# Performance work log

Hardware: AMD Instinct MI355X
Metric: run time of the kernel (lower is better)

## Reference

```python
import jax, jax.numpy as jnp
import numpy as np

B = 16384
IN_DIM = 1280
BELLY = 1024   # int(scale_dim * belly_expand)
SCALE = 512
NBINS = 100
NPAT = 10
TAU = 0.25
BASE = 3.0
LEVELS = 12


def setup_inputs() -> dict:
    key = jax.random.key(0)
    ks = jax.random.split(key, 10)
    def w(i, shape, fan_in):
        return jax.random.normal(ks[i], shape, jnp.float32) * (0.5 / np.sqrt(fan_in))
    return {
        "features": jax.random.normal(ks[0], (B, IN_DIM), jnp.float32),
        "timesteps": jax.random.randint(ks[1], (B,), 0, 1000, jnp.int32),
        "W1": w(2, (IN_DIM, BELLY), IN_DIM),
        "b1": jnp.zeros((BELLY,), jnp.float32),
        "W2": w(3, (BELLY, SCALE), BELLY),            # no bias (bias=False)
        "Wt": w(4, (SCALE, NBINS), SCALE),
        "bt": jnp.zeros((NBINS,), jnp.float32),
        "Wp": w(5, (SCALE, NBINS * NPAT), SCALE),
        "bp": jnp.zeros((NBINS * NPAT,), jnp.float32),
        "w_pos": w(6, (SCALE, 1), SCALE),             # cantor feature_to_position
        "b_pos": jnp.zeros((1,), jnp.float32),
        "alpha": jnp.float32(0.5),
    }


def cantor_staircase(z, positions, w_pos, b_pos, alpha):
    # z: [B, SCALE] normalized features; positions: [B] int timestep bins
    centers = jnp.array([0.5, 1.5, 2.5], jnp.float32)
    max_pos = positions.max() + 1
    denom = jnp.maximum(max_pos - 1, 1).astype(jnp.float32)
    pos_f = positions.astype(jnp.float32)
    x_base = jnp.where(max_pos > 1, pos_f / denom, pos_f)
    x_base = jnp.clip(x_base, 1e-6, 1.0 - 1e-6)
    shift = jnp.tanh((z @ w_pos)[:, 0] + b_pos[0]) * 0.3
    x0 = jnp.clip(x_base + shift, 1e-6, 1.0 - 1e-6)

    def step(carry, _):
        x, Cx, w = carry
        y = x * BASE                                   # [B]
        logits = -((y[:, None] - centers) ** 2) / (TAU + 1e-8)  # [B,3]
        p = jax.nn.softmax(logits, axis=-1)
        bit = p[:, 1] * alpha + p[:, 2]
        Cx = Cx + bit * w
        x = y - jnp.floor(y)
        return (x, Cx, w * 0.5), None

    (x, Cx, w), _ = jax.lax.scan(step, (x0, jnp.zeros_like(x0), jnp.float32(0.5)), None, length=LEVELS)
    return jnp.clip(Cx, 0.0, 1.0)


def reference(features, timesteps, W1, b1, W2, Wt, bt, Wp, bp, w_pos, b_pos, alpha):
    # projection: Linear -> ReLU -> (dropout=identity at eval) -> Linear(no bias)
    h = jax.nn.relu(features @ W1 + b1)                # [B, BELLY]
    z = h @ W2                                         # [B, SCALE]
    z = z / jnp.maximum(jnp.linalg.norm(z, axis=-1, keepdims=True), 1e-12)
    timestep_logits = z @ Wt + bt                      # [B, NBINS]
    timestep_class = jnp.clip(
        (timesteps.astype(jnp.float32) / 1000.0 * NBINS).astype(jnp.int32), 0, NBINS - 1)
    cantor_values = cantor_staircase(z, timestep_class, w_pos, b_pos, alpha)
    pattern_logits = z @ Wp + bp                       # [B, NBINS*NPAT]
    return (z, timestep_logits, pattern_logits, timestep_class, cantor_values)
```

## Files before the change

### kernel.cpp

```cpp
#include <hip/hip_runtime.h>

#define B_ROWS 16384
#define IN_DIM 1280
#define BELLY  1024
#define SCALE  512
#define NBINS  100
#define NPTOT  1000

typedef __attribute__((ext_vector_type(8))) short short8_t;
typedef __attribute__((ext_vector_type(4))) float f32x4;

__device__ __forceinline__ unsigned short f2bf(float f) {
  union { float f; unsigned int u; } v; v.f = f;
  unsigned int r = v.u + 0x7FFFu + ((v.u >> 16) & 1u);
  return (unsigned short)(r >> 16);
}

__device__ __forceinline__ void gload16(const void* g, void* l) {
  __builtin_amdgcn_global_load_lds(
      (const __attribute__((address_space(1))) unsigned int*)g,
      (__attribute__((address_space(3))) unsigned int*)l, 16, 0, 0);
}

__global__ void cvt_f32_bf16(const float* __restrict__ in,
                             unsigned short* __restrict__ out, int n4) {
  int i = blockIdx.x * blockDim.x + threadIdx.x;
  int stride = gridDim.x * blockDim.x;
  for (; i < n4; i += stride) {
    float4 v = ((const float4*)in)[i];
    ushort4 o;
    o.x = f2bf(v.x); o.y = f2bf(v.y); o.z = f2bf(v.z); o.w = f2bf(v.w);
    ((ushort4*)out)[i] = o;
  }
}

__global__ void transpose_cvt(const float* __restrict__ in,
                              unsigned short* __restrict__ out,
                              int K, int N, int Npad) {
  __shared__ float tile[32][33];
  int k0 = blockIdx.x * 32;
  int n0 = blockIdx.y * 32;
  int tx = threadIdx.x, ty = threadIdx.y;
  #pragma unroll
  for (int r = 0; r < 32; r += 8) {
    int k = k0 + ty + r, n = n0 + tx;
    tile[ty + r][tx] = (k < K && n < N) ? in[(size_t)k * N + n] : 0.0f;
  }
  __syncthreads();
  #pragma unroll
  for (int r = 0; r < 32; r += 8) {
    int n = n0 + ty + r, k = k0 + tx;
    if (n < Npad && k < K) out[(size_t)n * K + k] = f2bf(tile[tx][ty + r]);
  }
}

__global__ void tclass_kernel(const int* __restrict__ ts, float* __restrict__ outc,
                              int* __restrict__ gmax, int n) {
  __shared__ int smax;
  if (threadIdx.x == 0) smax = 0;
  __syncthreads();
  int local = 0;
  for (int i = blockIdx.x * blockDim.x + threadIdx.x; i < n;
       i += gridDim.x * blockDim.x) {
    float v = (float)ts[i] / 1000.0f * 100.0f;
    int c = (int)v;
    c = min(max(c, 0), NBINS - 1);
    outc[i] = (float)c;
    local = max(local, c);
  }
  atomicMax(&smax, local);
  __syncthreads();
  if (threadIdx.x == 0) atomicMax(gmax, smax);
}

template<int K, int EPI>
__global__ __launch_bounds__(512, 1)
void gemm256(const unsigned short* __restrict__ A,
             const unsigned short* __restrict__ Bt,
             float* __restrict__ outF, unsigned short* __restrict__ outH,
             const float* __restrict__ bias, int Nvalid, int ldOut) {
  __shared__ __align__(16) unsigned short lds[65536];
  constexpr int NT = K / 64;
  static_assert(NT % 2 == 0, "NT must be even");
  const int tid  = threadIdx.x;
  const int wid  = tid >> 6;
  const int lane = tid & 63;
  const int r0 = blockIdx.x * 256;
  const int c0 = blockIdx.y * 256;

  const int srow = wid * 16 + (lane >> 3);
  const int scol = (((lane & 7) ^ (lane >> 3)) << 3);
  const unsigned short* gA = A  + (size_t)(r0 + srow) * K + scol;
  const unsigned short* gB = Bt + (size_t)(c0 + srow) * K + scol;
  const int sdst = wid * 1024;

  const int fr = lane & 15;
  const int Ah = wid >> 2;
  const int wc = (wid & 3) * 64;
  const int ca0 = ((((lane >> 4) << 4) +  0) ^ ((lane & 7) << 4)) >> 1;
  const int ca1 = ((((lane >> 4) << 4) + 64) ^ ((lane & 7) << 4)) >> 1;

  f32x4 acc[8][4] = {};
  short8_t af[4][2];
  short8_t bfr[2][2][2];

#define STAGE_(buf, mat, half, kt) do {                                        \
    const unsigned short* g_ = ((mat) == 0 ? gA : gB)                          \
        + (size_t)(half) * 128 * K + (size_t)(kt) * 64;                        \
    unsigned short* l_ = &lds[(buf) * 32768 + (mat) * 16384 + (half) * 8192 + sdst]; \
    gload16(g_, l_);                                                           \
    gload16(g_ + 8 * K, l_ + 512);                                             \
  } while (0)

#define LDA_(buf, mh) do {                                                     \
    const unsigned short* ab_ = &lds[(buf) * 32768 + Ah * 8192];               \
    _Pragma("unroll")                                                          \
    for (int mm = 0; mm < 4; ++mm) {                                           \
      int rwh_ = (mh) * 64 + mm * 16 + fr;                                     \
      af[mm][0] = *(const short8_t*)&ab_[rwh_ * 64 + ca0];                     \
      af[mm][1] = *(const short8_t*)&ab_[rwh_ * 64 + ca1];                     \
    } } while (0)

#define LDB_(buf, nh) do {                                                     \
    _Pragma("unroll")                                                          \
    for (int nn = 0; nn < 2; ++nn) {                                           \
      int brow_ = wc + ((nh) * 2 + nn) * 16;                                   \
      const unsigned short* bb_ = &lds[(buf) * 32768 + 16384 + (brow_ >> 7) * 8192]; \
      int rwh_ = (brow_ & 127) + fr;                                           \
      bfr[nh][nn][0] = *(const short8_t*)&bb_[rwh_ * 64 + ca0];                \
      bfr[nh][nn][1] = *(const short8_t*)&bb_[rwh_ * 64 + ca1];                \
    } } while (0)

#define MM_(mh, nh) do {                                                       \
    _Pragma("unroll")                                                          \
    for (int mm = 0; mm < 4; ++mm)                                             \
      _Pragma("unroll")                                                        \
      for (int nn = 0; nn < 2; ++nn) {                                         \
        acc[(mh)*4+mm][(nh)*2+nn] = __builtin_amdgcn_mfma_f32_16x16x32_bf16(   \
            af[mm][0], bfr[nh][nn][0], acc[(mh)*4+mm][(nh)*2+nn], 0, 0, 0);    \
        acc[(mh)*4+mm][(nh)*2+nn] = __builtin_amdgcn_mfma_f32_16x16x32_bf16(   \
            af[mm][1], bfr[nh][nn][1], acc[(mh)*4+mm][(nh)*2+nn], 0, 0, 0);    \
      } } while (0)

#define BAR_       __builtin_amdgcn_s_barrier()
#define LGKM0_     asm volatile("s_waitcnt lgkmcnt(0)")
#define VM4_       asm volatile("s_waitcnt vmcnt(4)" ::: "memory")
#define PRIO1_     __builtin_amdgcn_s_setprio(1)
#define PRIO0_     __builtin_amdgcn_s_setprio(0)

  STAGE_(0, 1, 0, 0); STAGE_(0, 1, 1, 0);
  STAGE_(0, 0, 0, 0); STAGE_(0, 0, 1, 0);
  STAGE_(1, 1, 0, 1); STAGE_(1, 1, 1, 1);
  VM4_;
  BAR_;

  for (int t = 0; t < NT; t += 2) {
    const int t2 = (t + 2) % NT;
    const int t3 = (t + 3) % NT;
    LDA_(0, 0); LDB_(0, 0); STAGE_(1, 0, 0, t + 1);
    BAR_; LGKM0_; PRIO1_; MM_(0, 0); PRIO0_; BAR_;
    LDB_(0, 1); STAGE_(1, 0, 1, t + 1);
    BAR_; LGKM0_; PRIO1_; MM_(0, 1); PRIO0_; BAR_;
    LDA_(0, 1); STAGE_(0, 1, 0, t2);
    BAR_; LGKM0_; PRIO1_; MM_(1, 0); PRIO0_; BAR_;
    STAGE_(0, 1, 1, t2); VM4_;
    BAR_; LGKM0_; PRIO1_; MM_(1, 1); PRIO0_; BAR_;
    LDA_(1, 0); LDB_(1, 0); STAGE_(0, 0, 0, t2);
    BAR_; LGKM0_; PRIO1_; MM_(0, 0); PRIO0_; BAR_;
    LDB_(1, 1); STAGE_(0, 0, 1, t2);
    BAR_; LGKM0_; PRIO1_; MM_(0, 1); PRIO0_; BAR_;
    LDA_(1, 1); STAGE_(1, 1, 0, t3);
    BAR_; LGKM0_; PRIO1_; MM_(1, 0); PRIO0_; BAR_;
    STAGE_(1, 1, 1, t3); VM4_;
    BAR_; LGKM0_; PRIO1_; MM_(1, 1); PRIO0_; BAR_;
  }

  asm volatile("s_waitcnt vmcnt(0)" ::: "memory");

  const int orow = (lane >> 4) * 4;
  const int wrr  = (wid >> 2) * 128;
  #pragma unroll
  for (int m = 0; m < 8; ++m) {
    #pragma unroll
    for (int n = 0; n < 4; ++n) {
      #pragma unroll
      for (int i = 0; i < 4; ++i) {
        int row = r0 + wrr + m * 16 + orow + i;
        int col = c0 + wc + n * 16 + fr;
        float v = acc[m][n][i];
        if (EPI == 0) {
          v += bias[col];
          v = fmaxf(v, 0.0f);
          outH[(size_t)row * ldOut + col] = f2bf(v);
        } else if (EPI == 1) {
          outF[(size_t)row * ldOut + col] = v;
        } else {
          if (col < Nvalid) outF[(size_t)row * ldOut + col] = v + bias[col];
        }
      }
    }
  }
#undef STAGE_
#undef LDA_
#undef LDB_
#undef MM_
}

template<int K, int EPI>
__global__ __launch_bounds__(256)
void gemm128(const unsigned short* __restrict__ A,
             const unsigned short* __restrict__ Bt,
             float* __restrict__ outF, unsigned short* __restrict__ outH,
             const float* __restrict__ bias, int Nvalid, int ldOut) {
  __shared__ __align__(16) unsigned short As[128 * 32];
  __shared__ __align__(16) unsigned short Bs[128 * 32];

  const int tid  = threadIdx.x;
  const int wid  = tid >> 6;
  const int lane = tid & 63;
  const int r0 = blockIdx.x * 128;
  const int c0 = blockIdx.y * 128;

  const int arow = lane >> 2;
  const int acol = (lane & 3) * 8;
  const unsigned short* gA0 = A  + (size_t)(r0 + 16 * (2 * wid + 0) + arow) * K + acol;
  const unsigned short* gA1 = A  + (size_t)(r0 + 16 * (2 * wid + 1) + arow) * K + acol;
  const unsigned short* gB0 = Bt + (size_t)(c0 + 16 * (2 * wid + 0) + arow) * K + acol;
  const unsigned short* gB1 = Bt + (size_t)(c0 + 16 * (2 * wid + 1) + arow) * K + acol;
  unsigned short* lA0 = &As[(2 * wid + 0) * 512];
  unsigned short* lA1 = &As[(2 * wid + 1) * 512];
  unsigned short* lB0 = &Bs[(2 * wid + 0) * 512];
  unsigned short* lB1 = &Bs[(2 * wid + 1) * 512];

  const int wr   = (wid >> 1) * 64;
  const int wc   = (wid & 1) * 64;
  const int fr   = lane & 15;
  const int koff = (lane >> 4) * 8;

  f32x4 acc[4][4] = {};

  for (int k0 = 0; k0 < K; k0 += 32) {
    gload16(gA0 + k0, lA0);
    gload16(gA1 + k0, lA1);
    gload16(gB0 + k0, lB0);
    gload16(gB1 + k0, lB1);
    __syncthreads();

    short8_t af[4], bfr[4];
    #pragma unroll
    for (int m = 0; m < 4; ++m)
      af[m] = *(const short8_t*)&As[(wr + m * 16 + fr) * 32 + koff];
    #pragma unroll
    for (int n = 0; n < 4; ++n)
      bfr[n] = *(const short8_t*)&Bs[(wc + n * 16 + fr) * 32 + koff];

    #pragma unroll
    for (int m = 0; m < 4; ++m)
      #pragma unroll
      for (int n = 0; n < 4; ++n)
        acc[m][n] = __builtin_amdgcn_mfma_f32_16x16x32_bf16(af[m], bfr[n], acc[m][n], 0, 0, 0);

    __syncthreads();
  }

  const int orow = (lane >> 4) * 4;
  #pragma unroll
  for (int m = 0; m < 4; ++m) {
    #pragma unroll
    for (int n = 0; n < 4; ++n) {
      #pragma unroll
      for (int i = 0; i < 4; ++i) {
        int row = r0 + wr + m * 16 + orow + i;
        int col = c0 + wc + n * 16 + fr;
        float v = acc[m][n][i];
        if (EPI == 0) {
          v += bias[col];
          v = fmaxf(v, 0.0f);
          outH[(size_t)row * ldOut + col] = f2bf(v);
        } else if (EPI == 1) {
          outF[(size_t)row * ldOut + col] = v;
        } else {
          if (col < Nvalid) outF[(size_t)row * ldOut + col] = v + bias[col];
        }
      }
    }
  }
}

__global__ void normalize_kernel(const float* __restrict__ zraw,
                                 float* __restrict__ zout,
                                 unsigned short* __restrict__ zb) {
  int wid = threadIdx.x >> 6, lane = threadIdx.x & 63;
  int row = blockIdx.x * 4 + wid;
  const float4* zr = (const float4*)(zraw + (size_t)row * SCALE);
  float4 v0 = zr[lane];
  float4 v1 = zr[lane + 64];
  float s = v0.x * v0.x + v0.y * v0.y + v0.z * v0.z + v0.w * v0.w
          + v1.x * v1.x + v1.y * v1.y + v1.z * v1.z + v1.w * v1.w;
  #pragma unroll
  for (int off = 1; off < 64; off <<= 1) s += __shfl_xor(s, off);
  float scale = 1.0f / fmaxf(sqrtf(s), 1e-12f);
  float4 o0, o1;
  o0.x = v0.x * scale; o0.y = v0.y * scale; o0.z = v0.z * scale; o0.w = v0.w * scale;
  o1.x = v1.x * scale; o1.y = v1.y * scale; o1.z = v1.z * scale; o1.w = v1.w * scale;
  ((float4*)(zout + (size_t)row * SCALE))[lane] = o0;
  ((float4*)(zout + (size_t)row * SCALE))[lane + 64] = o1;
  ushort4 b0, b1;
  b0.x = f2bf(o0.x); b0.y = f2bf(o0.y); b0.z = f2bf(o0.z); b0.w = f2bf(o0.w);
  b1.x = f2bf(o1.x); b1.y = f2bf(o1.y); b1.z = f2bf(o1.z); b1.w = f2bf(o1.w);
  ((ushort4*)(zb + (size_t)row * SCALE))[lane] = b0;
  ((ushort4*)(zb + (size_t)row * SCALE))[lane + 64] = b1;
}

__global__ void cantor_kernel(const float* __restrict__ z,
                              const float* __restrict__ w_pos,
                              const float* __restrict__ b_pos,
                              const float* __restrict__ alpha_p,
                              const float* __restrict__ tclassf,
                              const int* __restrict__ gmax,
                              float* __restrict__ out) {
  int wid = threadIdx.x >> 6, lane = threadIdx.x & 63;
  int row = blockIdx.x * 4 + wid;
  const float4* zr = (const float4*)(z + (size_t)row * SCALE);
  const float4* wp = (const float4*)w_pos;
  float4 a0 = zr[lane], a1 = zr[lane + 64];
  float4 c0 = wp[lane], c1 = wp[lane + 64];
  float s = a0.x * c0.x + a0.y * c0.y + a0.z * c0.z + a0.w * c0.w
          + a1.x * c1.x + a1.y * c1.y + a1.z * c1.z + a1.w * c1.w;
  #pragma unroll
  for (int off = 1; off < 64; off <<= 1) s += __shfl_xor(s, off);

  float shift = tanhf(s + b_pos[0]) * 0.3f;
  int max_pos = *gmax + 1;
  float denom = (float)max(max_pos - 1, 1);
  float posf = tclassf[row];
  float x = (max_pos > 1) ? (posf / denom) : posf;
  x = fminf(fmaxf(x, 1e-6f), 1.0f - 1e-6f);
  x = x + shift;
  x = fminf(fmaxf(x, 1e-6f), 1.0f - 1e-6f);

  float alpha = alpha_p[0];
  const float inv = 1.0f / (0.25f + 1e-8f);
  float Cx = 0.0f, w = 0.5f;
  #pragma unroll
  for (int l = 0; l < 12; ++l) {
    float y = x * 3.0f;
    float d0 = y - 0.5f, d1 = y - 1.5f, d2 = y - 2.5f;
    float l0 = -(d0 * d0) * inv, l1 = -(d1 * d1) * inv, l2 = -(d2 * d2) * inv;
    float mx = fmaxf(l0, fmaxf(l1, l2));
    float e0 = __expf(l0 - mx), e1 = __expf(l1 - mx), e2 = __expf(l2 - mx);
    float bit = (e1 * alpha + e2) / (e0 + e1 + e2);
    Cx += bit * w;
    x = y - floorf(y);
    w *= 0.5f;
  }
  if (lane == 0) out[row] = fminf(fmaxf(Cx, 0.0f), 1.0f);
}

extern "C" void kernel_launch(void* const* d_in, const int* in_sizes, int n_in,
                              void* d_out, int out_size, void* d_ws, size_t ws_size,
                              hipStream_t stream) {
  const float* features = (const float*)d_in[0];
  const int*   timesteps = (const int*)d_in[1];
  const float* W1 = (const float*)d_in[2];
  const float* b1 = (const float*)d_in[3];
  const float* W2 = (const float*)d_in[4];
  const float* Wt = (const float*)d_in[5];
  const float* bt = (const float*)d_in[6];
  const float* Wp = (const float*)d_in[7];
  const float* bp = (const float*)d_in[8];
  const float* w_pos = (const float*)d_in[9];
  const float* b_pos = (const float*)d_in[10];
  const float* alpha = (const float*)d_in[11];

  char* ws = (char*)d_ws;
  const size_t WS_H   = (size_t)B_ROWS * IN_DIM * 2;
  const size_t WS_ZB  = WS_H + (size_t)B_ROWS * BELLY * 2;
  const size_t WS_W1T = WS_ZB + (size_t)B_ROWS * SCALE * 2;
  const size_t WS_W2T = WS_W1T + (size_t)BELLY * IN_DIM * 2;
  const size_t WS_WPT = WS_W2T + (size_t)SCALE * BELLY * 2;
  const size_t WS_WTT = WS_WPT + (size_t)1024 * SCALE * 2;
  const size_t WS_MAX = WS_WTT + (size_t)128 * SCALE * 2;

  unsigned short* featB = (unsigned short*)(ws);
  float*          zraw  = (float*)(ws);
  unsigned short* hB    = (unsigned short*)(ws + WS_H);
  unsigned short* zB    = (unsigned short*)(ws + WS_ZB);
  unsigned short* W1T   = (unsigned short*)(ws + WS_W1T);
  unsigned short* W2T   = (unsigned short*)(ws + WS_W2T);
  unsigned short* WPT   = (unsigned short*)(ws + WS_WPT);
  unsigned short* WTT   = (unsigned short*)(ws + WS_WTT);
  int*            gmax  = (int*)(ws + WS_MAX);

  float* out  = (float*)d_out;
  float* o_z  = out;
  float* o_t  = o_z + (size_t)B_ROWS * SCALE;
  float* o_p  = o_t + (size_t)B_ROWS * NBINS;
  float* o_c  = o_p + (size_t)B_ROWS * NPTOT;
  float* o_cv = o_c + B_ROWS;

  hipMemsetAsync(gmax, 0, 4, stream);

  cvt_f32_bf16<<<2048, 256, 0, stream>>>(features, featB, B_ROWS * IN_DIM / 4);

  dim3 tb(32, 8);
  transpose_cvt<<<dim3(40, 32), tb, 0, stream>>>(W1, W1T, IN_DIM, BELLY, BELLY);
  transpose_cvt<<<dim3(32, 16), tb, 0, stream>>>(W2, W2T, BELLY, SCALE, SCALE);
  transpose_cvt<<<dim3(16, 32), tb, 0, stream>>>(Wp, WPT, SCALE, NPTOT, 1024);
  transpose_cvt<<<dim3(16, 4),  tb, 0, stream>>>(Wt, WTT, SCALE, NBINS, 128);

  tclass_kernel<<<64, 256, 0, stream>>>(timesteps, o_c, gmax, B_ROWS);

  gemm256<IN_DIM, 0><<<dim3(B_ROWS / 256, BELLY / 256), 512, 0, stream>>>(
      featB, W1T, nullptr, hB, b1, BELLY, BELLY);
  gemm256<BELLY, 1><<<dim3(B_ROWS / 256, SCALE / 256), 512, 0, stream>>>(
      hB, W2T, zraw, nullptr, nullptr, SCALE, SCALE);

  normalize_kernel<<<B_ROWS / 4, 256, 0, stream>>>(zraw, o_z, zB);

  gemm256<SCALE, 2><<<dim3(B_ROWS / 256, 4), 512, 0, stream>>>(
      zB, WPT, o_p, nullptr, bp, NPTOT, NPTOT);
  gemm128<SCALE, 2><<<dim3(B_ROWS / 128, 1), 256, 0, stream>>>(
      zB, WTT, o_t, nullptr, bt, NBINS, NBINS);

  cantor_kernel<<<B_ROWS / 4, 256, 0, stream>>>(o_z, w_pos, b_pos, alpha, o_c, gmax, o_cv);
}
```

Baseline: 348.6 us.

## Fuse fp32->bf16 conversion into GEMM1, merge head GEMMs and norm+cantor

The first GEMM now loads fp32 features straight into registers, converts them to bf16 and writes them to LDS, which drops the separate conversion kernel and its bf16 round trip through memory. The Wp and Wt heads are combined into one transposed weight buffer so a single 5-column-tile GEMM writes both outputs, and gemm128 is removed. Normalization and the cantor computation are fused into one kernel that reuses the raw z dot product with w_pos. The risk is that register staging with vmcnt(0) waits may hurt pipelining in GEMM1, and the padded head columns waste some MFMA work.

```diff
diff --git a/kernel.cpp b/kernel.cpp
--- a/kernel.cpp
+++ b/kernel.cpp
@@ -1,4 +1,5 @@
 #include <hip/hip_runtime.h>
+#include <hip/hip_bf16.h>
 
 #define B_ROWS 16384
 #define IN_DIM 1280
@@ -20,18 +21,6 @@
   __builtin_amdgcn_global_load_lds(
       (const __attribute__((address_space(1))) unsigned int*)g,
       (__attribute__((address_space(3))) unsigned int*)l, 16, 0, 0);
-}
-
-__global__ void cvt_f32_bf16(const float* __restrict__ in,
-                             unsigned short* __restrict__ out, int n4) {
-  int i = blockIdx.x * blockDim.x + threadIdx.x;
-  int stride = gridDim.x * blockDim.x;
-  for (; i < n4; i += stride) {
-    float4 v = ((const float4*)in)[i];
-    ushort4 o;
-    o.x = f2bf(v.x); o.y = f2bf(v.y); o.z = f2bf(v.z); o.w = f2bf(v.w);
-    ((ushort4*)out)[i] = o;
-  }
 }
 
 __global__ void transpose_cvt(const float* __restrict__ in,
@@ -73,12 +62,14 @@
   if (threadIdx.x == 0) atomicMax(gmax, smax);
 }
 
-template<int K, int EPI>
+template<int K, int EPI, bool AF32>
 __global__ __launch_bounds__(512, 1)
-void gemm256(const unsigned short* __restrict__ A,
+void gemm256(const void* __restrict__ Av,
              const unsigned short* __restrict__ Bt,
              float* __restrict__ outF, unsigned short* __restrict__ outH,
-             const float* __restrict__ bias, int Nvalid, int ldOut) {
+             const float* __restrict__ bias,
+             float* __restrict__ outF2, const float* __restrict__ bias2,
+             int ldOut) {
   __shared__ __align__(16) unsigned short lds[65536];
   constexpr int NT = K / 64;
   static_assert(NT % 2 == 0, "NT must be even");
@@ -90,9 +81,14 @@
 
   const int srow = wid * 16 + (lane >> 3);
   const int scol = (((lane & 7) ^ (lane >> 3)) << 3);
-  const unsigned short* gA = A  + (size_t)(r0 + srow) * K + scol;
   const unsigned short* gB = Bt + (size_t)(c0 + srow) * K + scol;
+  const unsigned short* gA16 = AF32 ? nullptr
+      : (const unsigned short*)Av + (size_t)(r0 + srow) * K + scol;
+  const float* gAf = AF32
+      ? (const float*)Av + (size_t)(r0 + wid * 16 + (lane >> 3)) * K + (lane & 7) * 8
+      : nullptr;
   const int sdst = wid * 1024;
+  const int swzslot = (lane & 7) ^ (lane >> 3);
 
   const int fr = lane & 15;
   const int Ah = wid >> 2;
@@ -103,14 +99,46 @@
   f32x4 acc[8][4] = {};
   short8_t af[4][2];
   short8_t bfr[2][2][2];
-
-#define STAGE_(buf, mat, half, kt) do {                                        \
-    const unsigned short* g_ = ((mat) == 0 ? gA : gB)                          \
+  float av[2][2][8];
+
+#define STAGEB_(buf, half, kt) do {                                            \
+    const unsigned short* g_ = gB                                              \
         + (size_t)(half) * 128 * K + (size_t)(kt) * 64;                        \
-    unsigned short* l_ = &lds[(buf) * 32768 + (mat) * 16384 + (half) * 8192 + sdst]; \
+    unsigned short* l_ = &lds[(buf) * 32768 + 16384 + (half) * 8192 + sdst];   \
     gload16(g_, l_);                                                           \
     gload16(g_ + 8 * K, l_ + 512);                                             \
   } while (0)
+
+#define STAGEA16_(buf, half, kt) do {                                          \
+    const unsigned short* g_ = gA16                                            \
+        + (size_t)(half) * 128 * K + (size_t)(kt) * 64;                        \
+    unsigned short* l_ = &lds[(buf) * 32768 + (half) * 8192 + sdst];           \
+    gload16(g_, l_);                                                           \
+    gload16(g_ + 8 * K, l_ + 512);                                             \
+  } while (0)
+
+#define ALOAD_(kt) do {                                                        \
+    _Pragma("unroll")                                                          \
+    for (int h_ = 0; h_ < 2; ++h_)                                             \
+      _Pragma("unroll")                                                        \
+      for (int j_ = 0; j_ < 2; ++j_) {                                         \
+        const float* p_ = gAf + (size_t)(h_ * 128 + j_ * 8) * K + (size_t)(kt) * 64; \
+        *(float4*)&av[h_][j_][0] = ((const float4*)p_)[0];                     \
+        *(float4*)&av[h_][j_][4] = ((const float4*)p_)[1];                     \
+      } } while (0)
+
+#define AWRITE_(buf) do {                                                      \
+    asm volatile("s_waitcnt vmcnt(0)" ::: "memory");                           \
+    _Pragma("unroll")                                                          \
+    for (int h_ = 0; h_ < 2; ++h_)                                             \
+      _Pragma("unroll")                                                        \
+      for (int j_ = 0; j_ < 2; ++j_) {                                         \
+        union { short8_t v; unsigned short u[8]; } t_;                         \
+        _Pragma("unroll")                                                      \
+        for (int e_ = 0; e_ < 8; ++e_) t_.u[e_] = f2bf(av[h_][j_][e_]);        \
+        *(short8_t*)&lds[(buf) * 32768 + h_ * 8192 + sdst                      \
+                         + (lane >> 3) * 64 + j_ * 512 + swzslot * 8] = t_.v;  \
+      } } while (0)
 
 #define LDA_(buf, mh) do {                                                     \
     const unsigned short* ab_ = &lds[(buf) * 32768 + Ah * 8192];               \
@@ -148,31 +176,60 @@
 #define PRIO1_     __builtin_amdgcn_s_setprio(1)
 #define PRIO0_     __builtin_amdgcn_s_setprio(0)
 
-  STAGE_(0, 1, 0, 0); STAGE_(0, 1, 1, 0);
-  STAGE_(0, 0, 0, 0); STAGE_(0, 0, 1, 0);
-  STAGE_(1, 1, 0, 1); STAGE_(1, 1, 1, 1);
-  VM4_;
-  BAR_;
+  if constexpr (AF32) {
+    ALOAD_(0);
+    STAGEB_(0, 0, 0); STAGEB_(0, 1, 0);
+    STAGEB_(1, 0, 1); STAGEB_(1, 1, 1);
+    AWRITE_(0);
+    ALOAD_(1);
+    LGKM0_;
+    BAR_;
+  } else {
+    STAGEB_(0, 0, 0); STAGEB_(0, 1, 0);
+    STAGEA16_(0, 0, 0); STAGEA16_(0, 1, 0);
+    STAGEB_(1, 0, 1); STAGEB_(1, 1, 1);
+    VM4_;
+    BAR_;
+  }
 
   for (int t = 0; t < NT; t += 2) {
     const int t2 = (t + 2) % NT;
     const int t3 = (t + 3) % NT;
-    LDA_(0, 0); LDB_(0, 0); STAGE_(1, 0, 0, t + 1);
-    BAR_; LGKM0_; PRIO1_; MM_(0, 0); PRIO0_; BAR_;
-    LDB_(0, 1); STAGE_(1, 0, 1, t + 1);
-    BAR_; LGKM0_; PRIO1_; MM_(0, 1); PRIO0_; BAR_;
-    LDA_(0, 1); STAGE_(0, 1, 0, t2);
-    BAR_; LGKM0_; PRIO1_; MM_(1, 0); PRIO0_; BAR_;
-    STAGE_(0, 1, 1, t2); VM4_;
-    BAR_; LGKM0_; PRIO1_; MM_(1, 1); PRIO0_; BAR_;
-    LDA_(1, 0); LDB_(1, 0); STAGE_(0, 0, 0, t2);
-    BAR_; LGKM0_; PRIO1_; MM_(0, 0); PRIO0_; BAR_;
-    LDB_(1, 1); STAGE_(0, 0, 1, t2);
-    BAR_; LGKM0_; PRIO1_; MM_(0, 1); PRIO0_; BAR_;
-    LDA_(1, 1); STAGE_(1, 1, 0, t3);
-    BAR_; LGKM0_; PRIO1_; MM_(1, 0); PRIO0_; BAR_;
-    STAGE_(1, 1, 1, t3); VM4_;
-    BAR_; LGKM0_; PRIO1_; MM_(1, 1); PRIO0_; BAR_;
+    if constexpr (AF32) {
+      LDA_(0, 0); LDB_(0, 0);
+      BAR_; LGKM0_; PRIO1_; MM_(0, 0); PRIO0_; BAR_;
+      LDB_(0, 1); AWRITE_(1);
+      BAR_; LGKM0_; PRIO1_; MM_(0, 1); PRIO0_; BAR_;
+      LDA_(0, 1); STAGEB_(0, 0, t2); ALOAD_(t2);
+      BAR_; LGKM0_; PRIO1_; MM_(1, 0); PRIO0_; BAR_;
+      STAGEB_(0, 1, t2);
+      BAR_; LGKM0_; PRIO1_; MM_(1, 1); PRIO0_; BAR_;
+      LDA_(1, 0); LDB_(1, 0);
+      BAR_; LGKM0_; PRIO1_; MM_(0, 0); PRIO0_; BAR_;
+      LDB_(1, 1); AWRITE_(0);
+      BAR_; LGKM0_; PRIO1_; MM_(0, 1); PRIO0_; BAR_;
+      LDA_(1, 1); STAGEB_(1, 0, t3); ALOAD_(t3);
+      BAR_; LGKM0_; PRIO1_; MM_(1, 0); PRIO0_; BAR_;
+      STAGEB_(1, 1, t3);
+      BAR_; LGKM0_; PRIO1_; MM_(1, 1); PRIO0_; BAR_;
+    } else {
+      LDA_(0, 0); LDB_(0, 0); STAGEA16_(1, 0, t + 1);
+      BAR_; LGKM0_; PRIO1_; MM_(0, 0); PRIO0_; BAR_;
+      LDB_(0, 1); STAGEA16_(1, 1, t + 1);
+      BAR_; LGKM0_; PRIO1_; MM_(0, 1); PRIO0_; BAR_;
+      LDA_(0, 1); STAGEB_(0, 0, t2);
+      BAR_; LGKM0_; PRIO1_; MM_(1, 0); PRIO0_; BAR_;
+      STAGEB_(0, 1, t2); VM4_;
+      BAR_; LGKM0_; PRIO1_; MM_(1, 1); PRIO0_; BAR_;
+      LDA_(1, 0); LDB_(1, 0); STAGEA16_(0, 0, t2);
+      BAR_; LGKM0_; PRIO1_; MM_(0, 0); PRIO0_; BAR_;
+      LDB_(1, 1); STAGEA16_(0, 1, t2);
+      BAR_; LGKM0_; PRIO1_; MM_(0, 1); PRIO0_; BAR_;
+      LDA_(1, 1); STAGEB_(1, 0, t3);
+      BAR_; LGKM0_; PRIO1_; MM_(1, 0); PRIO0_; BAR_;
+      STAGEB_(1, 1, t3); VM4_;
+      BAR_; LGKM0_; PRIO1_; MM_(1, 1); PRIO0_; BAR_;
+    }
   }
 
   asm volatile("s_waitcnt vmcnt(0)" ::: "memory");
@@ -195,111 +252,52 @@
         } else if (EPI == 1) {
           outF[(size_t)row * ldOut + col] = v;
         } else {
-          if (col < Nvalid) outF[(size_t)row * ldOut + col] = v + bias[col];
+          if (col < NPTOT) {
+            outF[(size_t)row * ldOut + col] = v + bias[col];
+          } else if (col >= 1024) {
+            int cc = col - 1024;
+            if (cc < NBINS) outF2[(size_t)row * NBINS + cc] = v + bias2[cc];
+          }
         }
       }
     }
   }
-#undef STAGE_
+#undef STAGEB_
+#undef STAGEA16_
+#undef ALOAD_
+#undef AWRITE_
 #undef LDA_
 #undef LDB_
 #undef MM_
 }
 
-template<int K, int EPI>
-__global__ __launch_bounds__(256)
-void gemm128(const unsigned short* __restrict__ A,
-             const unsigned short* __restrict__ Bt,
-             float* __restrict__ outF, unsigned short* __restrict__ outH,
-             const float* __restrict__ bias, int Nvalid, int ldOut) {
-  __shared__ __align__(16) unsigned short As[128 * 32];
-  __shared__ __align__(16) unsigned short Bs[128 * 32];
-
-  const int tid  = threadIdx.x;
-  const int wid  = tid >> 6;
-  const int lane = tid & 63;
-  const int r0 = blockIdx.x * 128;
-  const int c0 = blockIdx.y * 128;
-
-  const int arow = lane >> 2;
-  const int acol = (lane & 3) * 8;
-  const unsigned short* gA0 = A  + (size_t)(r0 + 16 * (2 * wid + 0) + arow) * K + acol;
-  const unsigned short* gA1 = A  + (size_t)(r0 + 16 * (2 * wid + 1) + arow) * K + acol;
-  const unsigned short* gB0 = Bt + (size_t)(c0 + 16 * (2 * wid + 0) + arow) * K + acol;
-  const unsigned short* gB1 = Bt + (size_t)(c0 + 16 * (2 * wid + 1) + arow) * K + acol;
-  unsigned short* lA0 = &As[(2 * wid + 0) * 512];
-  unsigned short* lA1 = &As[(2 * wid + 1) * 512];
-  unsigned short* lB0 = &Bs[(2 * wid + 0) * 512];
-  unsigned short* lB1 = &Bs[(2 * wid + 1) * 512];
-
-  const int wr   = (wid >> 1) * 64;
-  const int wc   = (wid & 1) * 64;
-  const int fr   = lane & 15;
-  const int koff = (lane >> 4) * 8;
-
-  f32x4 acc[4][4] = {};
-
-  for (int k0 = 0; k0 < K; k0 += 32) {
-    gload16(gA0 + k0, lA0);
-    gload16(gA1 + k0, lA1);
-    gload16(gB0 + k0, lB0);
-    gload16(gB1 + k0, lB1);
-    __syncthreads();
-
-    short8_t af[4], bfr[4];
-    #pragma unroll
-    for (int m = 0; m < 4; ++m)
-      af[m] = *(const short8_t*)&As[(wr + m * 16 + fr) * 32 + koff];
-    #pragma unroll
-    for (int n = 0; n < 4; ++n)
-      bfr[n] = *(const short8_t*)&Bs[(wc + n * 16 + fr) * 32 + koff];
-
-    #pragma unroll
-    for (int m = 0; m < 4; ++m)
-      #pragma unroll
-      for (int n = 0; n < 4; ++n)
-        acc[m][n] = __builtin_amdgcn_mfma_f32_16x16x32_bf16(af[m], bfr[n], acc[m][n], 0, 0, 0);
-
-    __syncthreads();
-  }
-
-  const int orow = (lane >> 4) * 4;
-  #pragma unroll
-  for (int m = 0; m < 4; ++m) {
-    #pragma unroll
-    for (int n = 0; n < 4; ++n) {
-      #pragma unroll
-      for (int i = 0; i < 4; ++i) {
-        int row = r0 + wr + m * 16 + orow + i;
-        int col = c0 + wc + n * 16 + fr;
-        float v = acc[m][n][i];
-        if (EPI == 0) {
-          v += bias[col];
-          v = fmaxf(v, 0.0f);
-          outH[(size_t)row * ldOut + col] = f2bf(v);
-        } else if (EPI == 1) {
-          outF[(size_t)row * ldOut + col] = v;
-        } else {
-          if (col < Nvalid) outF[(size_t)row * ldOut + col] = v + bias[col];
-        }
-      }
-    }
-  }
-}
-
-__global__ void normalize_kernel(const float* __restrict__ zraw,
-                                 float* __restrict__ zout,
-                                 unsigned short* __restrict__ zb) {
+__global__ void norm_cantor_kernel(const float* __restrict__ zraw,
+                                   float* __restrict__ zout,
+                                   unsigned short* __restrict__ zb,
+                                   const float* __restrict__ w_pos,
+                                   const float* __restrict__ b_pos,
+                                   const float* __restrict__ alpha_p,
+                                   const float* __restrict__ tclassf,
+                                   const int* __restrict__ gmax,
+                                   float* __restrict__ cv_out) {
   int wid = threadIdx.x >> 6, lane = threadIdx.x & 63;
   int row = blockIdx.x * 4 + wid;
   const float4* zr = (const float4*)(zraw + (size_t)row * SCALE);
+  const float4* wp = (const float4*)w_pos;
   float4 v0 = zr[lane];
   float4 v1 = zr[lane + 64];
-  float s = v0.x * v0.x + v0.y * v0.y + v0.z * v0.z + v0.w * v0.w
-          + v1.x * v1.x + v1.y * v1.y + v1.z * v1.z + v1.w * v1.w;
+  float4 c0 = wp[lane];
+  float4 c1 = wp[lane + 64];
+  float ss = v0.x * v0.x + v0.y * v0.y + v0.z * v0.z + v0.w * v0.w
+           + v1.x * v1.x + v1.y * v1.y + v1.z * v1.z + v1.w * v1.w;
+  float rd = v0.x * c0.x + v0.y * c0.y + v0.z * c0.z + v0.w * c0.w
+           + v1.x * c1.x + v1.y * c1.y + v1.z * c1.z + v1.w * c1.w;
   #pragma unroll
-  for (int off = 1; off < 64; off <<= 1) s += __shfl_xor(s, off);
-  float scale = 1.0f / fmaxf(sqrtf(s), 1e-12f);
+  for (int off = 1; off < 64; off <<= 1) {
+    ss += __shfl_xor(ss, off);
+    rd += __shfl_xor(rd, off);
+  }
+  float scale = 1.0f / fmaxf(sqrtf(ss), 1e-12f);
   float4 o0, o1;
   o0.x = v0.x * scale; o0.y = v0.y * scale; o0.z = v0.z * scale; o0.w = v0.w * scale;
   o1.x = v1.x * scale; o1.y = v1.y * scale; o1.z = v1.z * scale; o1.w = v1.w * scale;
@@ -310,26 +308,8 @@
   b1.x = f2bf(o1.x); b1.y = f2bf(o1.y); b1.z = f2bf(o1.z); b1.w = f2bf(o1.w);
   ((ushort4*)(zb + (size_t)row * SCALE))[lane] = b0;
   ((ushort4*)(zb + (size_t)row * SCALE))[lane + 64] = b1;
-}
-
-__global__ void cantor_kernel(const float* __restrict__ z,
-                              const float* __restrict__ w_pos,
-                              const float* __restrict__ b_pos,
-                              const float* __restrict__ alpha_p,
-                              const float* __restrict__ tclassf,
-                              const int* __restrict__ gmax,
-                              float* __restrict__ out) {
-  int wid = threadIdx.x >> 6, lane = threadIdx.x & 63;
-  int row = blockIdx.x * 4 + wid;
-  const float4* zr = (const float4*)(z + (size_t)row * SCALE);
-  const float4* wp = (const float4*)w_pos;
-  float4 a0 = zr[lane], a1 = zr[lane + 64];
-  float4 c0 = wp[lane], c1 = wp[lane + 64];
-  float s = a0.x * c0.x + a0.y * c0.y + a0.z * c0.z + a0.w * c0.w
-          + a1.x * c1.x + a1.y * c1.y + a1.z * c1.z + a1.w * c1.w;
-  #pragma unroll
-  for (int off = 1; off < 64; off <<= 1) s += __shfl_xor(s, off);
-
+
+  float s = rd * scale;
   float shift = tanhf(s + b_pos[0]) * 0.3f;
   int max_pos = *gmax + 1;
   float denom = (float)max(max_pos - 1, 1);
@@ -354,7 +334,7 @@
     x = y - floorf(y);
     w *= 0.5f;
   }
-  if (lane == 0) out[row] = fminf(fmaxf(Cx, 0.0f), 1.0f);
+  if (lane == 0) cv_out[row] = fminf(fmaxf(Cx, 0.0f), 1.0f);
 }
 
 extern "C" void kernel_launch(void* const* d_in, const int* in_sizes, int n_in,
@@ -374,23 +354,20 @@
   const float* alpha = (const float*)d_in[11];
 
   char* ws = (char*)d_ws;
-  const size_t WS_H   = (size_t)B_ROWS * IN_DIM * 2;
-  const size_t WS_ZB  = WS_H + (size_t)B_ROWS * BELLY * 2;
+  const size_t WS_HB  = (size_t)B_ROWS * SCALE * 4;
+  const size_t WS_ZB  = WS_HB + (size_t)B_ROWS * BELLY * 2;
   const size_t WS_W1T = WS_ZB + (size_t)B_ROWS * SCALE * 2;
   const size_t WS_W2T = WS_W1T + (size_t)BELLY * IN_DIM * 2;
-  const size_t WS_WPT = WS_W2T + (size_t)SCALE * BELLY * 2;
-  const size_t WS_WTT = WS_WPT + (size_t)1024 * SCALE * 2;
-  const size_t WS_MAX = WS_WTT + (size_t)128 * SCALE * 2;
-
-  unsigned short* featB = (unsigned short*)(ws);
-  float*          zraw  = (float*)(ws);
-  unsigned short* hB    = (unsigned short*)(ws + WS_H);
-  unsigned short* zB    = (unsigned short*)(ws + WS_ZB);
-  unsigned short* W1T   = (unsigned short*)(ws + WS_W1T);
-  unsigned short* W2T   = (unsigned short*)(ws + WS_W2T);
-  unsigned short* WPT   = (unsigned short*)(ws + WS_WPT);
-  unsigned short* WTT   = (unsigned short*)(ws + WS_WTT);
-  int*            gmax  = (int*)(ws + WS_MAX);
+  const size_t WS_WCT = WS_W2T + (size_t)SCALE * BELLY * 2;
+  const size_t WS_MAX = WS_WCT + (size_t)1280 * SCALE * 2;
+
+  float*          zraw = (float*)(ws);
+  unsigned short* hB   = (unsigned short*)(ws + WS_HB);
+  unsigned short* zB   = (unsigned short*)(ws + WS_ZB);
+  unsigned short* W1T  = (unsigned short*)(ws + WS_W1T);
+  unsigned short* W2T  = (unsigned short*)(ws + WS_W2T);
+  unsigned short* WCT  = (unsigned short*)(ws + WS_WCT);
+  int*            gmax = (int*)(ws + WS_MAX);
 
   float* out  = (float*)d_out;
   float* o_z  = out;
@@ -401,27 +378,23 @@
 
   hipMemsetAsync(gmax, 0, 4, stream);
 
-  cvt_f32_bf16<<<2048, 256, 0, stream>>>(features, featB, B_ROWS * IN_DIM / 4);
-
   dim3 tb(32, 8);
   transpose_cvt<<<dim3(40, 32), tb, 0, stream>>>(W1, W1T, IN_DIM, BELLY, BELLY);
   transpose_cvt<<<dim3(32, 16), tb, 0, stream>>>(W2, W2T, BELLY, SCALE, SCALE);
-  transpose_cvt<<<dim3(16, 32), tb, 0, stream>>>(Wp, WPT, SCALE, NPTOT, 1024);
-  transpose_cvt<<<dim3(16, 4),  tb, 0, stream>>>(Wt, WTT, SCALE, NBINS, 128);
+  transpose_cvt<<<dim3(16, 32), tb, 0, stream>>>(Wp, WCT, SCALE, NPTOT, 1024);
+  transpose_cvt<<<dim3(16, 8),  tb, 0, stream>>>(Wt, WCT + (size_t)1024 * SCALE,
+                                                 SCALE, NBINS, 256);
 
   tclass_kernel<<<64, 256, 0, stream>>>(timesteps, o_c, gmax, B_ROWS);
 
-  gemm256<IN_DIM, 0><<<dim3(B_ROWS / 256, BELLY / 256), 512, 0, stream>>>(
-      featB, W1T, nullptr, hB, b1, BELLY, BELLY);
-  gemm256<BELLY, 1><<<dim3(B_ROWS / 256, SCALE / 256), 512, 0, stream>>>(
-      hB, W2T, zraw, nullptr, nullptr, SCALE, SCALE);
-
-  normalize_kernel<<<B_ROWS / 4, 256, 0, stream>>>(zraw, o_z, zB);
-
-  gemm256<SCALE, 2><<<dim3(B_ROWS / 256, 4), 512, 0, stream>>>(
-      zB, WPT, o_p, nullptr, bp, NPTOT, NPTOT);
-  gemm128<SCALE, 2><<<dim3(B_ROWS / 128, 1), 256, 0, stream>>>(
-      zB, WTT, o_t, nullptr, bt, NBINS, NBINS);
-
-  cantor_kernel<<<B_ROWS / 4, 256, 0, stream>>>(o_z, w_pos, b_pos, alpha, o_c, gmax, o_cv);
-}
+  gemm256<IN_DIM, 0, true><<<dim3(B_ROWS / 256, BELLY / 256), 512, 0, stream>>>(
+      features, W1T, nullptr, hB, b1, nullptr, nullptr, BELLY);
+  gemm256<BELLY, 1, false><<<dim3(B_ROWS / 256, SCALE / 256), 512, 0, stream>>>(
+      hB, W2T, zraw, nullptr, nullptr, nullptr, nullptr, SCALE);
+
+  norm_cantor_kernel<<<B_ROWS / 4, 256, 0, stream>>>(
+      zraw, o_z, zB, w_pos, b_pos, alpha, o_c, gmax, o_cv);
+
+  gemm256<SCALE, 2, false><<<dim3(B_ROWS / 256, 5), 512, 0, stream>>>(
+      zB, WCT, o_p, nullptr, bp, o_t, bt, NPTOT);
+}
```

Measured after the change: 386.7 us. +10.9%, slower.
